# Optimization experiments

Measured on AMD Instinct MI355X. Metric: run time of the kernel, lower is better.

The kernel has to match this reference:

```python
import jax, jax.numpy as jnp
import numpy as np

B = 8192          # number of analysis windows
N = 4096          # window_size (power of 2, matches radix-2 Cooley-Tukey)


def setup_inputs() -> dict:
    key = jax.random.key(0)
    x = jax.random.normal(key, (B, N), dtype=jnp.float32)
    return {"x": x}


def reference(x):
    """Power spectrum |F(k)|^2 per window.

    The original module implements an exact radix-2 DIT Cooley-Tukey FFT
    (bit-reversal permutation + log2(N) butterfly stages with twiddle
    factors exp(-2*pi*i*k/N)) and returns re^2 + im^2. That is exactly the
    unnormalized DFT, so the clean/efficient faithful form is jnp.fft.fft
    followed by squared magnitude, batched over the leading axis.
    """
    f = jnp.fft.fft(x.astype(jnp.complex64), axis=-1)  # [B, N] complex
    return (jnp.real(f) ** 2 + jnp.imag(f) ** 2).astype(x.dtype)  # [B, N]
```

## Files before the change

kernel.cpp:

```cpp
#include <hip/hip_runtime.h>
#include <math.h>

#define FFT_N   4096
#define NT      256
#define PHYS(i) ((i) + ((i) >> 4))
#define LDS_SZ  (FFT_N + FFT_N / 16)

__device__ __forceinline__ float2 cadd(float2 a, float2 b) { return make_float2(a.x + b.x, a.y + b.y); }
__device__ __forceinline__ float2 csub(float2 a, float2 b) { return make_float2(a.x - b.x, a.y - b.y); }
__device__ __forceinline__ float2 cmul(float2 a, float2 b) { return make_float2(a.x * b.x - a.y * b.y, a.x * b.y + a.y * b.x); }

__device__ __forceinline__ void dft4(float2& a, float2& b, float2& c, float2& d) {
    float2 t0 = cadd(a, c);
    float2 t1 = csub(a, c);
    float2 t2 = cadd(b, d);
    float2 t3 = make_float2(b.y - d.y, d.x - b.x);
    a = cadd(t0, t2);
    b = cadd(t1, t3);
    c = csub(t0, t2);
    d = csub(t1, t3);
}

__device__ __forceinline__ void dft16(float2 v[16]) {
    #pragma unroll
    for (int r1 = 0; r1 < 4; ++r1)
        dft4(v[r1], v[r1 + 4], v[r1 + 8], v[r1 + 12]);

    const float C1 = 0.92387953251128675613f;
    const float S1 = 0.38268343236508977173f;
    const float R2 = 0.70710678118654752440f;
    v[5]  = cmul(v[5],  make_float2( C1, -S1));
    v[9]  = cmul(v[9],  make_float2( R2, -R2));
    v[13] = cmul(v[13], make_float2( S1, -C1));
    v[6]  = cmul(v[6],  make_float2( R2, -R2));
    v[10] = make_float2(v[10].y, -v[10].x);
    v[14] = cmul(v[14], make_float2(-R2, -R2));
    v[7]  = cmul(v[7],  make_float2( S1, -C1));
    v[11] = cmul(v[11], make_float2(-R2, -R2));
    v[15] = cmul(v[15], make_float2(-C1,  S1));
    #pragma unroll
    for (int q1 = 0; q1 < 4; ++q1)
        dft4(v[4 * q1], v[4 * q1 + 1], v[4 * q1 + 2], v[4 * q1 + 3]);
}

template <int M>
__device__ __forceinline__ void store_stage_tw(float2* buf, int tid, float2 v[16]) {
    const int j = tid / M;
    const int k = tid % M;
    const int obase = j * 16 * M + k;
    float sn, cs;
    __sincosf((float)j * (-6.28318530717958647692f * (float)M / (float)FFT_N), &sn, &cs);
    float2 w[16];
    w[1]  = make_float2(cs, sn);
    w[2]  = cmul(w[1], w[1]);
    w[3]  = cmul(w[2], w[1]);
    w[4]  = cmul(w[2], w[2]);
    w[5]  = cmul(w[4], w[1]);
    w[6]  = cmul(w[4], w[2]);
    w[7]  = cmul(w[4], w[3]);
    w[8]  = cmul(w[4], w[4]);
    w[9]  = cmul(w[8], w[1]);
    w[10] = cmul(w[8], w[2]);
    w[11] = cmul(w[8], w[3]);
    w[12] = cmul(w[8], w[4]);
    w[13] = cmul(w[8], w[5]);
    w[14] = cmul(w[8], w[6]);
    w[15] = cmul(w[8], w[7]);
    buf[PHYS(obase)] = v[0];
    #pragma unroll
    for (int q = 1; q < 16; ++q) {
        const int reg = ((q & 3) << 2) | (q >> 2);
        buf[PHYS(obase + q * M)] = cmul(v[reg], w[q]);
    }
}

__device__ __forceinline__ void load_stage(const float2* buf, int tid, float2 v[16]) {
    #pragma unroll
    for (int r = 0; r < 16; ++r) v[r] = buf[PHYS(tid + 256 * r)];
}

__global__ __launch_bounds__(NT) void spec_fft_kernel(const float* __restrict__ x,
                                                      float* __restrict__ out) {
    __shared__ float2 buf[LDS_SZ];
    const int tid = threadIdx.x;
    const size_t base = (size_t)blockIdx.x * (2 * FFT_N);
    const float* __restrict__ x1 = x + base + tid;
    const float* __restrict__ x2 = x + base + FFT_N + tid;

    float2 v[16];
    #pragma unroll
    for (int r = 0; r < 16; ++r)
        v[r] = make_float2(x1[256 * r], x2[256 * r]);

    dft16(v);
    store_stage_tw<1>(buf, tid, v);
    __syncthreads();

    load_stage(buf, tid, v);
    __syncthreads();
    dft16(v);
    store_stage_tw<16>(buf, tid, v);
    __syncthreads();

    load_stage(buf, tid, v);
    __syncthreads();
    dft16(v);
    #pragma unroll
    for (int q = 0; q < 16; ++q) {
        const int reg = ((q & 3) << 2) | (q >> 2);
        buf[PHYS(tid + 256 * q)] = v[reg];
    }
    __syncthreads();

    float* __restrict__ o1 = out + base;
    float* __restrict__ o2 = out + base + FFT_N;
    #pragma unroll
    for (int q = 0; q < 16; ++q) {
        const int reg = ((q & 3) << 2) | (q >> 2);
        const int k = tid + 256 * q;
        float2 zk = v[reg];
        float2 zn = buf[PHYS((FFT_N - k) & (FFT_N - 1))];
        float e1r = zk.x + zn.x, e1i = zk.y - zn.y;
        float e2r = zk.x - zn.x, e2i = zk.y + zn.y;
        __builtin_nontemporal_store(0.25f * (e1r * e1r + e1i * e1i), o1 + k);
        __builtin_nontemporal_store(0.25f * (e2r * e2r + e2i * e2i), o2 + k);
    }
}

extern "C" void kernel_launch(void* const* d_in, const int* in_sizes, int n_in,
                              void* d_out, int out_size, void* d_ws, size_t ws_size,
                              hipStream_t stream) {
    const float* x = (const float*)d_in[0];
    float* out = (float*)d_out;
    const int B = in_sizes[0] / FFT_N;
    spec_fft_kernel<<<B / 2, NT, 0, stream>>>(x, out);
}
```

Before: 48.23 us.

## Exploit real-input spectral symmetry and use packed float2 vector math

Switches the complex arithmetic to clang ext_vector float2 types so the compiler can emit packed FP32 instructions. The output stage now relies on the power spectrum of real signals being symmetric: each thread computes bins k and N-k together, stores both, and writes only half the spectrum to LDS. Bin 2048 is handled separately by a single thread. This cuts LDS writes and reads in the final stage, at the cost of scattered reversed-index global stores and a serial tail on thread 0.

```diff
diff --git a/kernel.cpp b/kernel.cpp
--- a/kernel.cpp
+++ b/kernel.cpp
@@ -6,22 +6,25 @@
 #define PHYS(i) ((i) + ((i) >> 4))
 #define LDS_SZ  (FFT_N + FFT_N / 16)
 
-__device__ __forceinline__ float2 cadd(float2 a, float2 b) { return make_float2(a.x + b.x, a.y + b.y); }
-__device__ __forceinline__ float2 csub(float2 a, float2 b) { return make_float2(a.x - b.x, a.y - b.y); }
-__device__ __forceinline__ float2 cmul(float2 a, float2 b) { return make_float2(a.x * b.x - a.y * b.y, a.x * b.y + a.y * b.x); }
+typedef float f2 __attribute__((ext_vector_type(2)));
 
-__device__ __forceinline__ void dft4(float2& a, float2& b, float2& c, float2& d) {
-    float2 t0 = cadd(a, c);
-    float2 t1 = csub(a, c);
-    float2 t2 = cadd(b, d);
-    float2 t3 = make_float2(b.y - d.y, d.x - b.x);
-    a = cadd(t0, t2);
-    b = cadd(t1, t3);
-    c = csub(t0, t2);
-    d = csub(t1, t3);
+__device__ __forceinline__ f2 cmul(f2 a, f2 b) {
+    return (f2){a.x, a.x} * b + (f2){-a.y, a.y} * (f2){b.y, b.x};
 }
 
-__device__ __forceinline__ void dft16(float2 v[16]) {
+__device__ __forceinline__ void dft4(f2& a, f2& b, f2& c, f2& d) {
+    f2 t0 = a + c;
+    f2 t1 = a - c;
+    f2 t2 = b + d;
+    f2 s  = b - d;
+    f2 t3 = (f2){s.y, -s.x};
+    a = t0 + t2;
+    b = t1 + t3;
+    c = t0 - t2;
+    d = t1 - t3;
+}
+
+__device__ __forceinline__ void dft16(f2 v[16]) {
     #pragma unroll
     for (int r1 = 0; r1 < 4; ++r1)
         dft4(v[r1], v[r1 + 4], v[r1 + 8], v[r1 + 12]);
@@ -29,29 +32,29 @@
     const float C1 = 0.92387953251128675613f;
     const float S1 = 0.38268343236508977173f;
     const float R2 = 0.70710678118654752440f;
-    v[5]  = cmul(v[5],  make_float2( C1, -S1));
-    v[9]  = cmul(v[9],  make_float2( R2, -R2));
-    v[13] = cmul(v[13], make_float2( S1, -C1));
-    v[6]  = cmul(v[6],  make_float2( R2, -R2));
-    v[10] = make_float2(v[10].y, -v[10].x);
-    v[14] = cmul(v[14], make_float2(-R2, -R2));
-    v[7]  = cmul(v[7],  make_float2( S1, -C1));
-    v[11] = cmul(v[11], make_float2(-R2, -R2));
-    v[15] = cmul(v[15], make_float2(-C1,  S1));
+    v[5]  = cmul(v[5],  (f2){ C1, -S1});
+    v[9]  = cmul(v[9],  (f2){ R2, -R2});
+    v[13] = cmul(v[13], (f2){ S1, -C1});
+    v[6]  = cmul(v[6],  (f2){ R2, -R2});
+    v[10] = (f2){v[10].y, -v[10].x};
+    v[14] = cmul(v[14], (f2){-R2, -R2});
+    v[7]  = cmul(v[7],  (f2){ S1, -C1});
+    v[11] = cmul(v[11], (f2){-R2, -R2});
+    v[15] = cmul(v[15], (f2){-C1,  S1});
     #pragma unroll
     for (int q1 = 0; q1 < 4; ++q1)
         dft4(v[4 * q1], v[4 * q1 + 1], v[4 * q1 + 2], v[4 * q1 + 3]);
 }
 
 template <int M>
-__device__ __forceinline__ void store_stage_tw(float2* buf, int tid, float2 v[16]) {
+__device__ __forceinline__ void store_stage_tw(f2* buf, int tid, f2 v[16]) {
     const int j = tid / M;
     const int k = tid % M;
     const int obase = j * 16 * M + k;
     float sn, cs;
     __sincosf((float)j * (-6.28318530717958647692f * (float)M / (float)FFT_N), &sn, &cs);
-    float2 w[16];
-    w[1]  = make_float2(cs, sn);
+    f2 w[16];
+    w[1]  = (f2){cs, sn};
     w[2]  = cmul(w[1], w[1]);
     w[3]  = cmul(w[2], w[1]);
     w[4]  = cmul(w[2], w[2]);
@@ -74,56 +77,68 @@
     }
 }
 
-__device__ __forceinline__ void load_stage(const float2* buf, int tid, float2 v[16]) {
+__device__ __forceinline__ void load_stage(const f2* buf, int tid, f2 v[16]) {
     #pragma unroll
     for (int r = 0; r < 16; ++r) v[r] = buf[PHYS(tid + 256 * r)];
 }
 
 __global__ __launch_bounds__(NT) void spec_fft_kernel(const float* __restrict__ x,
                                                       float* __restrict__ out) {
-    __shared__ float2 buf[LDS_SZ];
-    const int tid = threadIdx.x;
+    __shared__ f2 buf[LDS_SZ];
+    const int t = threadIdx.x;
     const size_t base = (size_t)blockIdx.x * (2 * FFT_N);
-    const float* __restrict__ x1 = x + base + tid;
-    const float* __restrict__ x2 = x + base + FFT_N + tid;
+    const float* __restrict__ x1 = x + base + t;
+    const float* __restrict__ x2 = x + base + FFT_N + t;
 
-    float2 v[16];
+    f2 v[16];
     #pragma unroll
     for (int r = 0; r < 16; ++r)
-        v[r] = make_float2(x1[256 * r], x2[256 * r]);
+        v[r] = (f2){x1[256 * r], x2[256 * r]};
 
     dft16(v);
-    store_stage_tw<1>(buf, tid, v);
+    store_stage_tw<1>(buf, t, v);
     __syncthreads();
 
-    load_stage(buf, tid, v);
+    load_stage(buf, t, v);
     __syncthreads();
     dft16(v);
-    store_stage_tw<16>(buf, tid, v);
+    store_stage_tw<16>(buf, t, v);
     __syncthreads();
 
-    load_stage(buf, tid, v);
+    load_stage(buf, t, v);
     __syncthreads();
     dft16(v);
+    buf[PHYS(t)] = v[0];
     #pragma unroll
-    for (int q = 0; q < 16; ++q) {
+    for (int q = 8; q < 16; ++q) {
         const int reg = ((q & 3) << 2) | (q >> 2);
-        buf[PHYS(tid + 256 * q)] = v[reg];
+        buf[PHYS(t + 256 * q)] = v[reg];
     }
     __syncthreads();
 
     float* __restrict__ o1 = out + base;
     float* __restrict__ o2 = out + base + FFT_N;
     #pragma unroll
-    for (int q = 0; q < 16; ++q) {
+    for (int q = 0; q < 8; ++q) {
         const int reg = ((q & 3) << 2) | (q >> 2);
-        const int k = tid + 256 * q;
-        float2 zk = v[reg];
-        float2 zn = buf[PHYS((FFT_N - k) & (FFT_N - 1))];
-        float e1r = zk.x + zn.x, e1i = zk.y - zn.y;
-        float e2r = zk.x - zn.x, e2i = zk.y + zn.y;
-        __builtin_nontemporal_store(0.25f * (e1r * e1r + e1i * e1i), o1 + k);
-        __builtin_nontemporal_store(0.25f * (e2r * e2r + e2i * e2i), o2 + k);
+        const int k = t + 256 * q;
+        const int m = (FFT_N - k) & (FFT_N - 1);
+        f2 zk = v[reg];
+        f2 zn = buf[PHYS(m)];
+        f2 zc = (f2){zn.x, -zn.y};
+        f2 e1 = zk + zc;
+        f2 e2 = zk - zc;
+        float p1 = 0.25f * (e1.x * e1.x + e1.y * e1.y);
+        float p2 = 0.25f * (e2.x * e2.x + e2.y * e2.y);
+        __builtin_nontemporal_store(p1, o1 + k);
+        __builtin_nontemporal_store(p2, o2 + k);
+        __builtin_nontemporal_store(p1, o1 + m);
+        __builtin_nontemporal_store(p2, o2 + m);
+    }
+    if (t == 0) {
+        f2 z = buf[PHYS(2048)];
+        __builtin_nontemporal_store(z.x * z.x, o1 + 2048);
+        __builtin_nontemporal_store(z.y * z.y, o2 + 2048);
     }
 }
 
```

New measurement: 49.35 us. +2.3%, slower.
